# Kernel optimization log

Measured on AMD Instinct MI355X. Metric: run time of the kernel, lower is better.

Reference implementation:

```python
import jax, jax.numpy as jnp
import numpy as np

N_NODES = 50000
N_EDGES = 800000
F_NODE = 64
F_EDGE = 32
F_GLOBAL = 32
OUT_DIM = 64
N_GRAPHS = 256


def setup_inputs() -> dict:
    key = jax.random.key(0)
    ks = jax.random.split(key, 8)
    x = jax.random.normal(ks[0], (N_NODES, F_NODE), dtype=jnp.float32)
    edge_index = jax.random.randint(ks[1], (2, N_EDGES), 0, N_NODES, dtype=jnp.int64)
    edge_attr = jax.random.normal(ks[2], (N_EDGES, F_EDGE), dtype=jnp.float32)
    u = jax.random.normal(ks[3], (N_GRAPHS, F_GLOBAL), dtype=jnp.float32)
    batch = jnp.sort(jax.random.randint(ks[4], (N_NODES,), 0, N_GRAPHS, dtype=jnp.int64))
    # params (scaled like default Linear init)
    W1 = jax.random.normal(ks[5], (F_NODE + F_EDGE, OUT_DIM), dtype=jnp.float32) / np.sqrt(F_NODE + F_EDGE)
    b1 = jnp.zeros((OUT_DIM,), dtype=jnp.float32)
    W2 = jax.random.normal(ks[6], (F_NODE + OUT_DIM + F_GLOBAL, OUT_DIM), dtype=jnp.float32) / np.sqrt(F_NODE + OUT_DIM + F_GLOBAL)
    b2 = jnp.zeros((OUT_DIM,), dtype=jnp.float32)
    return {"x": x, "edge_index": edge_index, "edge_attr": edge_attr,
            "u": u, "batch": batch, "W1": W1, "b1": b1, "W2": W2, "b2": b2}


def reference(x, edge_index, edge_attr, u, batch, W1, b1, W2, b2):
    dest, src = edge_index[0], edge_index[1]
    # gather source node features + edge attrs -> [E, F_NODE + F_EDGE]
    edge_info = jnp.concatenate([x[src], edge_attr], axis=1)
    # node_mlp_1: Linear + ReLU
    edge_messages = jax.nn.relu(edge_info @ W1 + b1)  # [E, OUT_DIM]
    # scatter-sum into destination nodes
    aggregated = jax.ops.segment_sum(edge_messages, dest, num_segments=x.shape[0])  # [N, OUT_DIM]
    # concat node, aggregated messages, per-graph global
    node_info = jnp.concatenate([x, aggregated, u[batch]], axis=1)  # [N, F_NODE+OUT_DIM+F_GLOBAL]
    # node_mlp_2: Linear + ReLU
    return jax.nn.relu(node_info @ W2 + b2)  # [N, OUT_DIM]
```

## Files before the change

### kernel.cpp

```cpp
#include <hip/hip_runtime.h>
#include <hip/hip_bf16.h>
#include <hip/hip_fp16.h>

typedef __attribute__((ext_vector_type(8))) short short8;
typedef __attribute__((ext_vector_type(4))) float f32x4;
typedef __attribute__((ext_vector_type(4))) float floatv4;

constexpr int NN = 50000;
constexpr int NE = 800000;
constexpr int FN = 64;
constexpr int FE = 32;
constexpr int FG = 32;
constexpr int OD = 64;
constexpr int NG = 256;

constexpr int SCAN_B = 256;
constexpr int NBLK = (NN + SCAN_B - 1) / SCAN_B;

constexpr int NWIN_E = NE / 16;
constexpr int MS_BLOCKS = 2048;
constexpr int MS_WAVES  = MS_BLOCKS * 4;

constexpr int XCVT_BLOCKS = (NN * FN / 8 + 255) / 256;
constexpr int PRE_BLOCKS  = XCVT_BLOCKS + (NG * 64) / 256;

constexpr int NWIN_N = NN / 16;
constexpr int NODE_BLOCKS = 782;
constexpr int NODE_WAVES  = NODE_BLOCKS * 4;

static __device__ __forceinline__ unsigned pack_bf16(float a, float b) {
    __hip_bfloat162 h = __float22bfloat162_rn(float2{a, b});
    return *reinterpret_cast<unsigned*>(&h);
}

__global__ __launch_bounds__(256) void k_pre(const float* __restrict__ x,
                                             unsigned* __restrict__ xb32,
                                             const float* __restrict__ u,
                                             const float* __restrict__ W2,
                                             const float* __restrict__ b2,
                                             float* __restrict__ uW2b,
                                             int* __restrict__ cnt) {
    if (blockIdx.x >= XCVT_BLOCKS) {
        const int lane = threadIdx.x & 63;
        float wcol[FG];
#pragma unroll
        for (int k = 0; k < FG; ++k) wcol[k] = W2[(FN + OD + k) * OD + lane];
        const float bias = b2[lane];
        int g = ((blockIdx.x - XCVT_BLOCKS) * 256 + threadIdx.x) >> 6;
        g = __builtin_amdgcn_readfirstlane(g);
        if (g >= NG) return;
        const float* __restrict__ urow = u + (size_t)g * FG;
        float acc = bias;
#pragma unroll
        for (int k = 0; k < FG; ++k) acc = fmaf(urow[k], wcol[k], acc);
        uW2b[(size_t)g * OD + lane] = acc;
        return;
    }
    const int i = blockIdx.x * 256 + threadIdx.x;
    if (i < NN) cnt[i] = 0;
    if (i >= NN * FN / 8) return;
    const float4* p = (const float4*)(x + (size_t)i * 8);
    float4 f0 = p[0], f1 = p[1];
    uint4 o;
    o.x = pack_bf16(f0.x, f0.y);
    o.y = pack_bf16(f0.z, f0.w);
    o.z = pack_bf16(f1.x, f1.y);
    o.w = pack_bf16(f1.z, f1.w);
    ((uint4*)xb32)[i] = o;
}

__global__ __launch_bounds__(256) void k_hist(const int* __restrict__ ei,
                                              int* __restrict__ cnt) {
    const int e = blockIdx.x * blockDim.x + threadIdx.x;
    if (e < NE) atomicAdd(&cnt[ei[e]], 1);
}

__global__ __launch_bounds__(SCAN_B) void k_scan1(const int* __restrict__ cnt,
                                                  int* __restrict__ start,
                                                  int* __restrict__ bsum) {
    __shared__ int lds[SCAN_B];
    const int i = blockIdx.x * SCAN_B + threadIdx.x;
    const int v = (i < NN) ? cnt[i] : 0;
    lds[threadIdx.x] = v;
    __syncthreads();
#pragma unroll
    for (int off = 1; off < SCAN_B; off <<= 1) {
        int t = (threadIdx.x >= off) ? lds[threadIdx.x - off] : 0;
        __syncthreads();
        lds[threadIdx.x] += t;
        __syncthreads();
    }
    const int incl = lds[threadIdx.x];
    if (i < NN) start[i] = incl - v;
    if (threadIdx.x == SCAN_B - 1) bsum[blockIdx.x] = incl;
}

__global__ __launch_bounds__(SCAN_B) void k_scan23(int* __restrict__ start,
                                                   const int* __restrict__ bsum,
                                                   const int* __restrict__ cnt,
                                                   int* __restrict__ cursor) {
    __shared__ int lds[SCAN_B];
    const int t = threadIdx.x;
    lds[t] = (t < NBLK) ? bsum[t] : 0;
    __syncthreads();
#pragma unroll
    for (int off = 1; off < SCAN_B; off <<= 1) {
        int tv = (t >= off) ? lds[t - off] : 0;
        __syncthreads();
        lds[t] += tv;
        __syncthreads();
    }
    const int boff = (blockIdx.x == 0) ? 0 : lds[blockIdx.x - 1];

    const int i = blockIdx.x * SCAN_B + t;
    if (i < NN) {
        const int s = start[i] + boff;
        start[i] = s;
        cursor[i] = s;
        if (i == NN - 1) start[NN] = s + cnt[i];
    }
}

__global__ __launch_bounds__(256) void k_msgscat(const int* __restrict__ ei,
                                                 const float* __restrict__ ea,
                                                 const unsigned short* __restrict__ xb,
                                                 const float* __restrict__ W1,
                                                 const float* __restrict__ b1,
                                                 int* __restrict__ cursor,
                                                 unsigned short* __restrict__ mbuf) {
    const int l = threadIdx.x & 63;
    const int g = l >> 4;
    const int c = l & 15;

    short8 wf[3][4];
#pragma unroll
    for (int t = 0; t < 3; ++t)
#pragma unroll
        for (int b = 0; b < 4; ++b)
#pragma unroll
            for (int i = 0; i < 8; i += 2) {
                const int k = 32 * t + 8 * g + i;
                const unsigned p = pack_bf16(W1[k * OD + (c + 16 * b)],
                                             W1[(k + 1) * OD + (c + 16 * b)]);
                ((unsigned*)&wf[t][b])[i / 2] = p;
            }
    float bias[4];
#pragma unroll
    for (int b = 0; b < 4; ++b) bias[b] = b1[c + 16 * b];

    int wv = (blockIdx.x * blockDim.x + threadIdx.x) >> 6;
    wv = __builtin_amdgcn_readfirstlane(wv);

    for (int w = wv; w < NWIN_E; w += MS_WAVES) {
        const int e = w * 16 + c;
        const int dst = __builtin_nontemporal_load(&ei[e]);
        const int src = __builtin_nontemporal_load(&ei[NE + e]);
        int pos = 0;
        if (l < 16) pos = atomicAdd(&cursor[dst], 1);

        short8 a0, a1, a2;
        {
            const uint4* xr = (const uint4*)(xb + (size_t)src * FN);
            uint4 q0 = xr[g];
            uint4 q1 = xr[4 + g];
            a0 = *(short8*)&q0;
            a1 = *(short8*)&q1;
        }
        {
            const floatv4* er = (const floatv4*)(ea + (size_t)e * FE);
            floatv4 e0 = __builtin_nontemporal_load(&er[2 * g]);
            floatv4 e1 = __builtin_nontemporal_load(&er[2 * g + 1]);
            uint4 q2;
            q2.x = pack_bf16(e0.x, e0.y);
            q2.y = pack_bf16(e0.z, e0.w);
            q2.z = pack_bf16(e1.x, e1.y);
            q2.w = pack_bf16(e1.z, e1.w);
            a2 = *(short8*)&q2;
        }

        f32x4 accb[4];
#pragma unroll
        for (int b = 0; b < 4; ++b) {
            f32x4 acc = {0.f, 0.f, 0.f, 0.f};
            acc = __builtin_amdgcn_mfma_f32_16x16x32_bf16(a0, wf[0][b], acc, 0, 0, 0);
            acc = __builtin_amdgcn_mfma_f32_16x16x32_bf16(a1, wf[1][b], acc, 0, 0, 0);
            acc = __builtin_amdgcn_mfma_f32_16x16x32_bf16(a2, wf[2][b], acc, 0, 0, 0);
            accb[b] = acc;
        }

#pragma unroll
        for (int q = 0; q < 4; ++q) {
            const int pr = __shfl(pos, 4 * g + q);
            const float v0 = fmaxf(accb[0][q] + bias[0], 0.0f);
            const float v1 = fmaxf(accb[1][q] + bias[1], 0.0f);
            const float v2 = fmaxf(accb[2][q] + bias[2], 0.0f);
            const float v3 = fmaxf(accb[3][q] + bias[3], 0.0f);
            const __half2 h01 = __float22half2_rn(float2{v0, v1});
            const __half2 h23 = __float22half2_rn(float2{v2, v3});
            unsigned long long outv =
                ((unsigned long long)*reinterpret_cast<const unsigned*>(&h23) << 32) |
                (unsigned long long)*reinterpret_cast<const unsigned*>(&h01);
            __builtin_nontemporal_store(
                outv, reinterpret_cast<unsigned long long*>(mbuf + (size_t)pr * 64 + c * 4));
        }
    }
}

__global__ __launch_bounds__(256) void k_nodem2(const unsigned short* __restrict__ xb,
                                                const unsigned short* __restrict__ mbuf,
                                                const int* __restrict__ start,
                                                const int* __restrict__ bat,
                                                const float* __restrict__ uW2b,
                                                const float* __restrict__ W2,
                                                float* __restrict__ out) {
    const int l = threadIdx.x & 63;
    const int g = l >> 4;
    const int c = l & 15;

    short8 wf[4][4];
#pragma unroll
    for (int t = 0; t < 4; ++t)
#pragma unroll
        for (int b = 0; b < 4; ++b)
#pragma unroll
            for (int i = 0; i < 8; i += 2) {
                const int col = c + 16 * b;
                unsigned p;
                if (t < 2) {
                    const int k = 32 * t + 8 * g + i;
                    p = pack_bf16(W2[k * OD + col], W2[(k + 1) * OD + col]);
                } else {
                    const int sc0 = 32 * (t - 2) + 8 * g + i;
                    const int sc1 = sc0 + 1;
                    const int k0 = FN + ((sc0 >> 2) + 16 * (sc0 & 3));
                    const int k1 = FN + ((sc1 >> 2) + 16 * (sc1 & 3));
                    p = pack_bf16(W2[k0 * OD + col], W2[k1 * OD + col]);
                }
                ((unsigned*)&wf[t][b])[i / 2] = p;
            }

    int wv = (blockIdx.x * blockDim.x + threadIdx.x) >> 6;
    wv = __builtin_amdgcn_readfirstlane(wv);

    for (int w = wv; w < NWIN_N; w += NODE_WAVES) {
        const int n0 = w * 16;
        const int n = n0 + c;
        const int s0 = start[n];
        const int cntn = start[n + 1] - s0;

        int mc = cntn;
        mc = max(mc, __shfl_xor(mc, 1));
        mc = max(mc, __shfl_xor(mc, 2));
        mc = max(mc, __shfl_xor(mc, 4));
        mc = max(mc, __shfl_xor(mc, 8));

        float s2v[8] = {0, 0, 0, 0, 0, 0, 0, 0};
        float s3v[8] = {0, 0, 0, 0, 0, 0, 0, 0};
        const unsigned short* rowb = mbuf + (size_t)s0 * 64 + 8 * g;
        for (int i = 0; i < mc; ++i) {
            if (i < cntn) {
                const uint4 u2 = *(const uint4*)(rowb + (size_t)i * 64);
                const uint4 u3 = *(const uint4*)(rowb + (size_t)i * 64 + 32);
                const __half2* h2 = (const __half2*)&u2;
                const __half2* h3 = (const __half2*)&u3;
#pragma unroll
                for (int j = 0; j < 4; ++j) {
                    const float2 f2 = __half22float2(h2[j]);
                    const float2 f3 = __half22float2(h3[j]);
                    s2v[2 * j]     += f2.x;
                    s2v[2 * j + 1] += f2.y;
                    s3v[2 * j]     += f3.x;
                    s3v[2 * j + 1] += f3.y;
                }
            }
        }
        uint4 qa2, qa3;
        qa2.x = pack_bf16(s2v[0], s2v[1]);
        qa2.y = pack_bf16(s2v[2], s2v[3]);
        qa2.z = pack_bf16(s2v[4], s2v[5]);
        qa2.w = pack_bf16(s2v[6], s2v[7]);
        qa3.x = pack_bf16(s3v[0], s3v[1]);
        qa3.y = pack_bf16(s3v[2], s3v[3]);
        qa3.z = pack_bf16(s3v[4], s3v[5]);
        qa3.w = pack_bf16(s3v[6], s3v[7]);

        const uint4* xr = (const uint4*)(xb + (size_t)n * FN);
        uint4 qx0 = xr[g], qx1 = xr[4 + g];
        short8 a0 = *(short8*)&qx0, a1 = *(short8*)&qx1;
        short8 a2 = *(short8*)&qa2, a3 = *(short8*)&qa3;

        int bq[4];
#pragma unroll
        for (int q = 0; q < 4; ++q) bq[q] = bat[n0 + g * 4 + q];

#pragma unroll
        for (int b = 0; b < 4; ++b) {
            f32x4 acc = {0.f, 0.f, 0.f, 0.f};
            acc = __builtin_amdgcn_mfma_f32_16x16x32_bf16(a0, wf[0][b], acc, 0, 0, 0);
            acc = __builtin_amdgcn_mfma_f32_16x16x32_bf16(a1, wf[1][b], acc, 0, 0, 0);
            acc = __builtin_amdgcn_mfma_f32_16x16x32_bf16(a2, wf[2][b], acc, 0, 0, 0);
            acc = __builtin_amdgcn_mfma_f32_16x16x32_bf16(a3, wf[3][b], acc, 0, 0, 0);
#pragma unroll
            for (int q = 0; q < 4; ++q) {
                const int nn = n0 + g * 4 + q;
                const float val = acc[q] + uW2b[(size_t)bq[q] * OD + c + 16 * b];
                out[(size_t)nn * OD + c + 16 * b] = fmaxf(val, 0.0f);
            }
        }
    }
}

extern "C" void kernel_launch(void* const* d_in, const int* in_sizes, int n_in,
                              void* d_out, int out_size, void* d_ws, size_t ws_size,
                              hipStream_t stream) {
    const float* x    = (const float*)d_in[0];
    const int*   ei   = (const int*)d_in[1];
    const float* ea   = (const float*)d_in[2];
    const float* u    = (const float*)d_in[3];
    const int*   bat  = (const int*)d_in[4];
    const float* W1   = (const float*)d_in[5];
    const float* b1   = (const float*)d_in[6];
    const float* W2   = (const float*)d_in[7];
    const float* b2   = (const float*)d_in[8];
    float* out = (float*)d_out;

    char* ws = (char*)d_ws;
    auto alloc = [&](size_t bytes) {
        char* p = ws;
        ws += (bytes + 255) & ~size_t(255);
        return p;
    };
    unsigned short* xb = (unsigned short*)alloc((size_t)NN * FN * 2);
    float* uW2b    = (float*)alloc((size_t)NG * OD * sizeof(float));
    int*   cnt     = (int*)alloc((size_t)NN * sizeof(int));
    int*   start   = (int*)alloc((size_t)(NN + 1) * sizeof(int));
    int*   cursor  = (int*)alloc((size_t)NN * sizeof(int));
    int*   bsum    = (int*)alloc((size_t)NBLK * sizeof(int));
    unsigned short* mbuf = (unsigned short*)alloc((size_t)NE * OD * 2);

    k_pre<<<dim3(PRE_BLOCKS), dim3(256), 0, stream>>>(x, (unsigned*)xb, u, W2, b2, uW2b, cnt);

    k_hist<<<dim3((NE + 255) / 256), dim3(256), 0, stream>>>(ei, cnt);
    k_scan1<<<dim3(NBLK), dim3(SCAN_B), 0, stream>>>(cnt, start, bsum);
    k_scan23<<<dim3(NBLK), dim3(SCAN_B), 0, stream>>>(start, bsum, cnt, cursor);

    k_msgscat<<<dim3(MS_BLOCKS), dim3(256), 0, stream>>>(ei, ea, xb, W1, b1, cursor, mbuf);

    k_nodem2<<<dim3(NODE_BLOCKS), dim3(256), 0, stream>>>(xb, mbuf, start, bat, uW2b, W2, out);
}
```

Measured before the change: 172.1 us.

## Fuse histogram into pre kernel, single-block scan, memset counts, plain stores

```diff
diff --git a/kernel.cpp b/kernel.cpp
--- a/kernel.cpp
+++ b/kernel.cpp
@@ -14,15 +14,17 @@
 constexpr int OD = 64;
 constexpr int NG = 256;
 
-constexpr int SCAN_B = 256;
-constexpr int NBLK = (NN + SCAN_B - 1) / SCAN_B;
-
 constexpr int NWIN_E = NE / 16;
 constexpr int MS_BLOCKS = 2048;
 constexpr int MS_WAVES  = MS_BLOCKS * 4;
 
 constexpr int XCVT_BLOCKS = (NN * FN / 8 + 255) / 256;
-constexpr int PRE_BLOCKS  = XCVT_BLOCKS + (NG * 64) / 256;
+constexpr int UW2_BLOCKS  = (NG * 64) / 256;
+constexpr int HIST_BLOCKS = (NE + 255) / 256;
+constexpr int PRE_BLOCKS  = XCVT_BLOCKS + UW2_BLOCKS + HIST_BLOCKS;
+
+constexpr int SCAN_T   = 1024;
+constexpr int SCAN_PER = (NN + SCAN_T - 1) / SCAN_T;
 
 constexpr int NWIN_N = NN / 16;
 constexpr int NODE_BLOCKS = 782;
@@ -39,7 +41,13 @@
                                              const float* __restrict__ W2,
                                              const float* __restrict__ b2,
                                              float* __restrict__ uW2b,
+                                             const int* __restrict__ ei,
                                              int* __restrict__ cnt) {
+    if (blockIdx.x >= XCVT_BLOCKS + UW2_BLOCKS) {
+        const int e = (blockIdx.x - XCVT_BLOCKS - UW2_BLOCKS) * 256 + threadIdx.x;
+        if (e < NE) atomicAdd(&cnt[ei[e]], 1);
+        return;
+    }
     if (blockIdx.x >= XCVT_BLOCKS) {
         const int lane = threadIdx.x & 63;
         float wcol[FG];
@@ -57,7 +65,6 @@
         return;
     }
     const int i = blockIdx.x * 256 + threadIdx.x;
-    if (i < NN) cnt[i] = 0;
     if (i >= NN * FN / 8) return;
     const float4* p = (const float4*)(x + (size_t)i * 8);
     float4 f0 = p[0], f1 = p[1];
@@ -69,55 +76,34 @@
     ((uint4*)xb32)[i] = o;
 }
 
-__global__ __launch_bounds__(256) void k_hist(const int* __restrict__ ei,
-                                              int* __restrict__ cnt) {
-    const int e = blockIdx.x * blockDim.x + threadIdx.x;
-    if (e < NE) atomicAdd(&cnt[ei[e]], 1);
-}
-
-__global__ __launch_bounds__(SCAN_B) void k_scan1(const int* __restrict__ cnt,
-                                                  int* __restrict__ start,
-                                                  int* __restrict__ bsum) {
-    __shared__ int lds[SCAN_B];
-    const int i = blockIdx.x * SCAN_B + threadIdx.x;
-    const int v = (i < NN) ? cnt[i] : 0;
-    lds[threadIdx.x] = v;
+__global__ __launch_bounds__(SCAN_T) void k_scan(const int* __restrict__ cnt,
+                                                 int* __restrict__ start,
+                                                 int* __restrict__ cursor) {
+    __shared__ int lds[SCAN_T];
+    const int t = threadIdx.x;
+    const int i0 = t * SCAN_PER;
+    const int i1 = (i0 + SCAN_PER < NN) ? (i0 + SCAN_PER) : NN;
+
+    int s = 0;
+    for (int i = i0; i < i1; ++i) s += cnt[i];
+    lds[t] = s;
     __syncthreads();
 #pragma unroll
-    for (int off = 1; off < SCAN_B; off <<= 1) {
-        int t = (threadIdx.x >= off) ? lds[threadIdx.x - off] : 0;
+    for (int off = 1; off < SCAN_T; off <<= 1) {
+        int v = (t >= off) ? lds[t - off] : 0;
         __syncthreads();
-        lds[threadIdx.x] += t;
+        lds[t] += v;
         __syncthreads();
     }
-    const int incl = lds[threadIdx.x];
-    if (i < NN) start[i] = incl - v;
-    if (threadIdx.x == SCAN_B - 1) bsum[blockIdx.x] = incl;
-}
-
-__global__ __launch_bounds__(SCAN_B) void k_scan23(int* __restrict__ start,
-                                                   const int* __restrict__ bsum,
-                                                   const int* __restrict__ cnt,
-                                                   int* __restrict__ cursor) {
-    __shared__ int lds[SCAN_B];
-    const int t = threadIdx.x;
-    lds[t] = (t < NBLK) ? bsum[t] : 0;
-    __syncthreads();
-#pragma unroll
-    for (int off = 1; off < SCAN_B; off <<= 1) {
-        int tv = (t >= off) ? lds[t - off] : 0;
-        __syncthreads();
-        lds[t] += tv;
-        __syncthreads();
-    }
-    const int boff = (blockIdx.x == 0) ? 0 : lds[blockIdx.x - 1];
-
-    const int i = blockIdx.x * SCAN_B + t;
-    if (i < NN) {
-        const int s = start[i] + boff;
-        start[i] = s;
-        cursor[i] = s;
-        if (i == NN - 1) start[NN] = s + cnt[i];
+    const int excl = lds[t] - s;
+    if (t == SCAN_T - 1) start[NN] = lds[t];
+
+    int run = excl;
+    for (int i = i0; i < i1; ++i) {
+        const int v = cnt[i];
+        start[i] = run;
+        cursor[i] = run;
+        run += v;
     }
 }
 
@@ -197,11 +183,10 @@
             const float v3 = fmaxf(accb[3][q] + bias[3], 0.0f);
             const __half2 h01 = __float22half2_rn(float2{v0, v1});
             const __half2 h23 = __float22half2_rn(float2{v2, v3});
-            unsigned long long outv =
-                ((unsigned long long)*reinterpret_cast<const unsigned*>(&h23) << 32) |
-                (unsigned long long)*reinterpret_cast<const unsigned*>(&h01);
-            __builtin_nontemporal_store(
-                outv, reinterpret_cast<unsigned long long*>(mbuf + (size_t)pr * 64 + c * 4));
+            uint2 outv;
+            outv.x = *reinterpret_cast<const unsigned*>(&h01);
+            outv.y = *reinterpret_cast<const unsigned*>(&h23);
+            *reinterpret_cast<uint2*>(mbuf + (size_t)pr * 64 + c * 4) = outv;
         }
     }
 }
@@ -335,14 +320,14 @@
     int*   cnt     = (int*)alloc((size_t)NN * sizeof(int));
     int*   start   = (int*)alloc((size_t)(NN + 1) * sizeof(int));
     int*   cursor  = (int*)alloc((size_t)NN * sizeof(int));
-    int*   bsum    = (int*)alloc((size_t)NBLK * sizeof(int));
     unsigned short* mbuf = (unsigned short*)alloc((size_t)NE * OD * 2);
 
-    k_pre<<<dim3(PRE_BLOCKS), dim3(256), 0, stream>>>(x, (unsigned*)xb, u, W2, b2, uW2b, cnt);
-
-    k_hist<<<dim3((NE + 255) / 256), dim3(256), 0, stream>>>(ei, cnt);
-    k_scan1<<<dim3(NBLK), dim3(SCAN_B), 0, stream>>>(cnt, start, bsum);
-    k_scan23<<<dim3(NBLK), dim3(SCAN_B), 0, stream>>>(start, bsum, cnt, cursor);
+    hipMemsetAsync(cnt, 0, (size_t)NN * sizeof(int), stream);
+
+    k_pre<<<dim3(PRE_BLOCKS), dim3(256), 0, stream>>>(x, (unsigned*)xb, u, W2, b2,
+                                                      uW2b, ei, cnt);
+
+    k_scan<<<dim3(1), dim3(SCAN_T), 0, stream>>>(cnt, start, cursor);
 
     k_msgscat<<<dim3(MS_BLOCKS), dim3(256), 0, stream>>>(ei, ea, xb, W1, b1, cursor, mbuf);
 
```

Result: slower. 263.2 us (+53.0%).
